# Optimization experiments

Hardware: AMD Instinct MI355X
Metric: run time of the kernel (lower is better)

Reference implementation:

```python
import jax, jax.numpy as jnp
import numpy as np


def _fps(xyz, S):
    """Farthest point sampling over one cloud. xyz: [N,3] -> idx [S] (int32).
    Deterministic start at index 0 (torch_cluster.fps uses a random start; the
    algorithm is otherwise identical)."""
    d0 = jnp.sum((xyz - xyz[0]) ** 2, axis=-1)  # squared dist to first pick

    def step(mind, _):
        nxt = jnp.argmax(mind)                              # farthest from selected set
        d = jnp.sum((xyz - xyz[nxt]) ** 2, axis=-1)
        return jnp.minimum(mind, d), nxt.astype(jnp.int32)

    _, rest = jax.lax.scan(step, d0, None, length=S - 1)
    return jnp.concatenate([jnp.zeros((1,), jnp.int32), rest])


def _gather(points, idx):
    """points [B,N,C], idx [B,...] -> [B,...,C] (per-batch fancy gather)."""
    return jax.vmap(lambda p, i: p[i])(points, idx)


def setup_inputs() -> dict:
    key = jax.random.key(0)
    k1, k2 = jax.random.split(key)
    B, N, C = 8, 4096, 64
    channel_out = C + 3  # use_xyz=True
    return {
        "xyz": jax.random.normal(k1, (B, N, 3), dtype=jnp.float32),
        "points": jax.random.normal(k2, (B, N, C), dtype=jnp.float32),
        "affine_alpha": jnp.ones((1, 1, 1, channel_out), dtype=jnp.float32),
        "affine_beta": jnp.zeros((1, 1, 1, channel_out), dtype=jnp.float32),
        "groups": 1024,
        "kneighbors": 32,
    }


def reference(xyz, points, affine_alpha, affine_beta, groups, kneighbors):
    B, N, _ = xyz.shape
    S, K = groups, kneighbors

    # --- FPS sample S centroids per batch ---
    fps_idx = jax.vmap(lambda x: _fps(x, S))(xyz)              # [B,S]
    new_xyz = _gather(xyz, fps_idx)                            # [B,S,3]
    new_points = _gather(points, fps_idx)                      # [B,S,C]

    # --- KNN: K nearest input points for each centroid ---
    # squared distances [B,S,N] via ||q||^2 + ||x||^2 - 2 q.x
    d2 = (jnp.sum(new_xyz ** 2, -1)[..., None]
          + jnp.sum(xyz ** 2, -1)[:, None, :]
          - 2.0 * jnp.einsum("bsc,bnc->bsn", new_xyz, xyz))
    idx = jax.lax.top_k(-d2, K)[1]                             # [B,S,K]

    grouped_xyz = _gather(xyz, idx)                            # [B,S,K,3]
    grouped_points = _gather(points, idx)                      # [B,S,K,C]
    grouped_points = jnp.concatenate([grouped_points, grouped_xyz], axis=-1)  # use_xyz

    # --- per-group center normalize + global (per-batch) std, affine ---
    mean = jnp.mean(grouped_points, axis=2, keepdims=True)     # [B,S,1,C+3]
    centered = grouped_points - mean
    std = jnp.std(centered.reshape(B, -1), axis=-1, ddof=1)    # unbiased, like torch.std
    std = std[:, None, None, None]
    grouped_points = centered / (std + 1e-5)
    grouped_points = affine_alpha * grouped_points + affine_beta

    new_points_out = jnp.concatenate(
        [grouped_points,
         jnp.broadcast_to(new_points[:, :, None, :], (B, S, K, new_points.shape[-1]))],
        axis=-1)                                               # [B,S,K,2C+3]
    return new_xyz, new_points_out
```

## Files before the change

kernel.cpp:

```cpp
#include <hip/hip_runtime.h>
#include <math.h>

#define NPTS 4096
#define NS 1024
#define NK 32
#define NC 64
#define NCG 67
#define NCOUT 131
#define NB 8
#define GRID 512

typedef float v2f __attribute__((ext_vector_type(2)));
typedef unsigned long long ull;

__device__ __forceinline__ float wave_max_dpp(float v) {
  int x = __float_as_int(v);
#define DPP_STEP(ctrl)                                                        \
  {                                                                           \
    int t = __builtin_amdgcn_update_dpp(x, x, ctrl, 0xF, 0xF, false);         \
    x = __float_as_int(fmaxf(__int_as_float(x), __int_as_float(t)));          \
  }
  DPP_STEP(0x111)
  DPP_STEP(0x112)
  DPP_STEP(0x114)
  DPP_STEP(0x118)
  DPP_STEP(0x142)
  DPP_STEP(0x143)
#undef DPP_STEP
  return __int_as_float(__builtin_amdgcn_readlane(x, 63));
}

__device__ __forceinline__ void wave_argmin_dpp(float& v, int& i) {
#define ARG_STEP(ctrl)                                                         \
  {                                                                            \
    int tv = __builtin_amdgcn_update_dpp(__float_as_int(v), __float_as_int(v), \
                                         ctrl, 0xF, 0xF, false);               \
    int ti = __builtin_amdgcn_update_dpp(i, i, ctrl, 0xF, 0xF, false);         \
    float ov = __int_as_float(tv);                                             \
    bool t = (ov < v) || (ov == v && ti < i);                                  \
    v = t ? ov : v;                                                            \
    i = t ? ti : i;                                                            \
  }
  ARG_STEP(0x111) ARG_STEP(0x112) ARG_STEP(0x114)
  ARG_STEP(0x118) ARG_STEP(0x142) ARG_STEP(0x143)
#undef ARG_STEP
  v = __int_as_float(__builtin_amdgcn_readlane(__float_as_int(v), 63));
  i = __builtin_amdgcn_readlane(i, 63);
}

__device__ __forceinline__ void lds_barrier() {
  asm volatile("s_waitcnt lgkmcnt(0)" ::: "memory");
  __builtin_amdgcn_s_barrier();
  asm volatile("" ::: "memory");
}

__device__ __forceinline__ void unpack4(const float4* __restrict__ X4,
                                        float* px, float* py, float* pz) {
  float4 a = X4[0], c = X4[1], e = X4[2];
  px[0] = a.x; py[0] = a.y; pz[0] = a.z;
  px[1] = a.w; py[1] = c.x; pz[1] = c.y;
  px[2] = c.z; py[2] = c.w; pz[2] = e.x;
  px[3] = e.y; py[3] = e.z; pz[3] = e.w;
}

__device__ __forceinline__ void unpack16(const float4* __restrict__ X4,
                                         float* px, float* py, float* pz) {
#pragma unroll
  for (int g = 0; g < 4; ++g) unpack4(X4 + 3 * g, px + 4 * g, py + 4 * g, pz + 4 * g);
}

__global__ __launch_bounds__(256) void fused_kernel(const float* __restrict__ xyz,
                                                    const float* __restrict__ points,
                                                    float* __restrict__ newxyz,
                                                    int* __restrict__ fps_idx,
                                                    int* __restrict__ knn_idx,
                                                    float* __restrict__ mean_ws,
                                                    float* __restrict__ part_ws,
                                                    int* pick_idx) {
  __shared__ float4 coords4[NPTS];
  __shared__ int fps_lds[NS];
  __shared__ ull keys[2][4];
  __shared__ float pvv[2][4];
  __shared__ int pii[2][4];
  __shared__ int idx_lds[NK];
  __shared__ float red[256];
  __shared__ int gi_sh;

  const int tid = threadIdx.x;
  const int lane = tid & 63;
  const int wav = tid >> 6;
  const int bx = blockIdx.x;

  if (bx < NB) {
#pragma clang fp contract(off)
    __builtin_amdgcn_s_setprio(3);
    const int b = bx;
    const float* X = xyz + (size_t)b * NPTS * 3;
    const int base = tid * 16;
    float px[16], py[16], pz[16];
    unpack16((const float4*)(X + (size_t)base * 3), px, py, pz);
#pragma unroll
    for (int j = 0; j < 16; ++j) coords4[base + j] = make_float4(px[j], py[j], pz[j], 0.0f);
    v2f px2[8], py2[8], pz2[8], mind2[8];
#pragma unroll
    for (int q = 0; q < 8; ++q) {
      px2[q] = v2f{px[2 * q], px[2 * q + 1]};
      py2[q] = v2f{py[2 * q], py[2 * q + 1]};
      pz2[q] = v2f{pz[2 * q], pz[2 * q + 1]};
      mind2[q] = v2f{__builtin_inff(), __builtin_inff()};
    }
    float cx = X[0], cy = X[1], cz = X[2];
    int gi = 0;
    if (tid == 0) fps_lds[0] = 0;
    __syncthreads();

    for (int s = 1; s < NS; ++s) {
      v2f cxv = v2f{cx, cx}, cyv = v2f{cy, cy}, czv = v2f{cz, cz};
      v2f runmax = v2f{-1.0f, -1.0f};
#pragma unroll
      for (int q = 0; q < 8; ++q) {
        v2f dx = px2[q] - cxv;
        v2f dy = py2[q] - cyv;
        v2f dz = pz2[q] - czv;
        v2f d = ((dx * dx) + (dy * dy)) + (dz * dz);
        v2f m = __builtin_elementwise_min(mind2[q], d);
        mind2[q] = m;
        runmax = __builtin_elementwise_max(runmax, m);
      }
      float bv = fmaxf(runmax.x, runmax.y);
      int bj = 0;
#pragma unroll
      for (int q = 7; q >= 0; --q) {
        bj = (mind2[q].y == bv) ? 2 * q + 1 : bj;
        bj = (mind2[q].x == bv) ? 2 * q : bj;
      }
      float smax = wave_max_dpp(bv);
      ull lm = __ballot(bv == smax);
      int wl = (int)(__ffsll(lm) - 1);
      int bjw = __builtin_amdgcn_readlane(bj, wl);
      int gidx = ((wav << 6) + wl) * 16 + bjw;
      ull key = ((ull)__float_as_uint(smax) << 32) |
                (ull)(0xFFFFFFFFu - (unsigned)gidx);
      const int p = s & 1;
      if (lane == 0) keys[p][wav] = key;
      lds_barrier();
      ull k0 = keys[p][0], k1 = keys[p][1], k2 = keys[p][2], k3 = keys[p][3];
      ull ka = k0 > k1 ? k0 : k1;
      ull kb = k2 > k3 ? k2 : k3;
      ull km = ka > kb ? ka : kb;
      gi = (int)(0xFFFFFFFFu - (unsigned)(km & 0xFFFFFFFFull));
      float4 c4 = coords4[gi];
      if (tid == 0) {
        fps_lds[s] = gi;
        __hip_atomic_store(&pick_idx[b * NS + s], gi, __ATOMIC_RELAXED,
                           __HIP_MEMORY_SCOPE_AGENT);
      }
      cx = c4.x; cy = c4.y; cz = c4.z;
    }
    __syncthreads();
    for (int s = tid; s < NS; s += 256) {
      int g2 = fps_lds[s];
      float4 c4 = coords4[g2];
      fps_idx[b * NS + s] = g2;
      newxyz[(size_t)(b * NS + s) * 3 + 0] = c4.x;
      newxyz[(size_t)(b * NS + s) * 3 + 1] = c4.y;
      newxyz[(size_t)(b * NS + s) * 3 + 2] = c4.z;
    }
  } else {
    if (bx >= 256 && bx < 256 + NB) return;
    const int w = (bx < 256) ? (bx - NB) : (bx - NB - NB);
    const int nwork = GRID - 2 * NB;
    for (int q = w; q < NB * NS; q += nwork) {
      const int b = q & 7;
      const int s = q >> 3;
      const int bs = (b << 10) | s;
      int gi = 0;
      if (s != 0) {
        if (tid == 0) {
          int g = __hip_atomic_load(&pick_idx[bs], __ATOMIC_RELAXED,
                                    __HIP_MEMORY_SCOPE_AGENT);
          while (g == -1) {
            __builtin_amdgcn_s_sleep(64);
            g = __hip_atomic_load(&pick_idx[bs], __ATOMIC_RELAXED,
                                  __HIP_MEMORY_SCOPE_AGENT);
          }
          gi_sh = g;
        }
        __syncthreads();
        gi = gi_sh;
      }
      const float* X = xyz + (size_t)b * NPTS * 3;
      const float sx = X[gi * 3 + 0];
      const float sy = X[gi * 3 + 1];
      const float sz = X[gi * 3 + 2];
      const float snorm = __fadd_rn(__fadd_rn(__fmul_rn(sx, sx), __fmul_rn(sy, sy)),
                                    __fmul_rn(sz, sz));
      const int base = tid * 16;
      const float4* X4 = (const float4*)(X + (size_t)base * 3);
      float d2[16];
      float bv = __builtin_inff(); int bi = 0x7fffffff;
#pragma unroll
      for (int g4 = 0; g4 < 4; ++g4) {
        float qx[4], qy[4], qz[4];
        unpack4(X4 + 3 * g4, qx, qy, qz);
#pragma unroll
        for (int j = 0; j < 4; ++j) {
          const int jj = 4 * g4 + j;
          float nn = __fadd_rn(__fadd_rn(__fmul_rn(qx[j], qx[j]), __fmul_rn(qy[j], qy[j])),
                               __fmul_rn(qz[j], qz[j]));
          float dt = __fmaf_rn(sz, qz[j], __fmaf_rn(sy, qy[j], __fmul_rn(sx, qx[j])));
          float d = __fsub_rn(__fadd_rn(snorm, nn), __fmul_rn(2.0f, dt));
          d2[jj] = d;
          if (d < bv) { bv = d; bi = base + jj; }
        }
      }
      float wv = bv; int wi = bi;
      wave_argmin_dpp(wv, wi);
      for (int k = 0; k < NK; ++k) {
        const int p = k & 1;
        if ((tid & 63) == 0) { pvv[p][wav] = wv; pii[p][wav] = wi; }
        __syncthreads();
        float gv = pvv[p][0]; int g2 = pii[p][0];
#pragma unroll
        for (int ww = 1; ww < 4; ++ww) {
          float ov = pvv[p][ww]; int oi = pii[p][ww];
          bool t = (ov < gv) || (ov == gv && oi < g2);
          if (t) { gv = ov; g2 = oi; }
        }
        if (tid == 0) idx_lds[k] = g2;
        if ((g2 >> 10) == wav) {
          if ((g2 >> 4) == tid) {
            bv = __builtin_inff(); bi = 0x7fffffff;
#pragma unroll
            for (int j = 0; j < 16; ++j) {
              float d = d2[j];
              if (base + j == g2) { d = __builtin_inff(); d2[j] = d; }
              if (d < bv) { bv = d; bi = base + j; }
            }
          }
          wv = bv; wi = bi;
          wave_argmin_dpp(wv, wi);
        }
      }
      __syncthreads();
      if (tid < NK) knn_idx[(size_t)bs * NK + tid] = idx_lds[tid];
      float acc = 0.0f;
      if (tid < NCG) {
        const float* Pb = points + (size_t)b * NPTS * NC;
        const float* Xb = xyz + (size_t)b * NPTS * 3;
        float sum = 0.0f, sumsq = 0.0f;
#pragma unroll
        for (int k = 0; k < NK; ++k) {
          int row = idx_lds[k];
          float g = (tid < NC) ? Pb[(size_t)row * NC + tid] : Xb[(size_t)row * 3 + (tid - NC)];
          sum += g;
          sumsq = __fmaf_rn(g, g, sumsq);
        }
        float m = sum * (1.0f / 32.0f);
        mean_ws[(size_t)bs * NCG + tid] = m;
        acc = __fmaf_rn(-m, sum, sumsq);
      }
      red[tid] = acc;
      __syncthreads();
      for (int off = 128; off > 0; off >>= 1) {
        if (tid < off) red[tid] += red[tid + off];
        __syncthreads();
      }
      if (tid == 0) part_ws[bs] = red[0];
      __syncthreads();
    }
  }
}

__global__ __launch_bounds__(256) void scale_kernel(const float* __restrict__ part_ws,
                                                    float* __restrict__ scale_ws) {
  const int b = blockIdx.x;
  const int tid = threadIdx.x;
  __shared__ float red[256];
  const float* p = part_ws + (size_t)b * NS;
  float a = p[tid] + p[tid + 256] + p[tid + 512] + p[tid + 768];
  red[tid] = a;
  __syncthreads();
  for (int off = 128; off > 0; off >>= 1) {
    if (tid < off) red[tid] += red[tid + off];
    __syncthreads();
  }
  if (tid == 0) {
    float var = red[0] / 2195455.0f;
    scale_ws[b] = 1.0f / (sqrtf(var) + 1e-5f);
  }
}

__global__ __launch_bounds__(256) void out_kernel(const float* __restrict__ xyz,
                                                  const float* __restrict__ points,
                                                  const float* __restrict__ alpha,
                                                  const float* __restrict__ beta,
                                                  const int* __restrict__ fps_idx,
                                                  const int* __restrict__ knn_idx,
                                                  const float* __restrict__ mean_ws,
                                                  const float* __restrict__ scale_ws,
                                                  float* __restrict__ out2) {
  const int bs = blockIdx.x;
  const int b = bs >> 10;
  const int tid = threadIdx.x;
  __shared__ int idx[NK];
  __shared__ float mrow[NCG], al[NCG], be[NCG];
  __shared__ int fr_s;
  if (tid < NK) idx[tid] = knn_idx[(size_t)bs * NK + tid];
  if (tid < NCG) {
    mrow[tid] = mean_ws[(size_t)bs * NCG + tid];
    al[tid] = alpha[tid];
    be[tid] = beta[tid];
  }
  if (tid == 0) fr_s = fps_idx[bs];
  __syncthreads();
  const float scl = scale_ws[b];
  const int fr = fr_s;
  const float* Pb = points + (size_t)b * NPTS * NC;
  const float* Xb = xyz + (size_t)b * NPTS * 3;
  float* orow = out2 + (size_t)bs * NK * NCOUT;
  const float* Fr = Pb + (size_t)fr * NC;
  for (int e4 = tid; e4 < NK * NCOUT / 4; e4 += 256) {
    float4 v4;
    float* vp = &v4.x;
#pragma unroll
    for (int j = 0; j < 4; ++j) {
      int e = 4 * e4 + j;
      int k = e / NCOUT;
      int c = e - k * NCOUT;
      float v;
      if (c < NCG) {
        int row = idx[k];
        float gv = (c < NC) ? Pb[(size_t)row * NC + c] : Xb[(size_t)row * 3 + (c - NC)];
        v = (gv - mrow[c]) * scl * al[c] + be[c];
      } else {
        v = Fr[c - NCG];
      }
      vp[j] = v;
    }
    ((float4*)orow)[e4] = v4;
  }
}

extern "C" void kernel_launch(void* const* d_in, const int* in_sizes, int n_in,
                              void* d_out, int out_size, void* d_ws, size_t ws_size,
                              hipStream_t stream) {
  const float* xyz    = (const float*)d_in[0];
  const float* points = (const float*)d_in[1];
  const float* alpha  = (const float*)d_in[2];
  const float* beta   = (const float*)d_in[3];

  float* out = (float*)d_out;
  float* newxyz = out;
  float* out2 = out + (size_t)NB * NS * 3;

  char* ws = (char*)d_ws;
  int*   fps_idx  = (int*)(ws + 0);
  int*   knn_idx  = (int*)(ws + 32768);
  float* mean_ws  = (float*)(ws + 1081344);
  float* part_ws  = (float*)(ws + 3276800);
  float* scale_ws = (float*)(ws + 3309568);
  int*   pick_idx = (int*)(ws + 3309632);

  hipMemsetAsync(pick_idx, 0xFF, NB * NS * sizeof(int), stream);

  fused_kernel<<<GRID,    256, 0, stream>>>(xyz, points, newxyz, fps_idx, knn_idx,
                                            mean_ws, part_ws, pick_idx);
  scale_kernel<<<NB,      256, 0, stream>>>(part_ws, scale_ws);
  out_kernel  <<<NB * NS, 256, 0, stream>>>(xyz, points, alpha, beta, fps_idx, knn_idx,
                                            mean_ws, scale_ws, out2);
}
```

Before: 663.1 us.

## Replace per-step FPS workgroup barrier with tagged LDS key polling

Inside the serial FPS loop, the s_barrier after each wave publishes its argmax key is replaced by polling of the four LDS key slots. A parity tag bit in each key marks which iteration wrote it, so waves only wait for the data they need instead of a full workgroup barrier. The gather worker mapping also skips blocks 8-15, presumably to keep more CUs or slots free near the FPS blocks. The spin loop depends on relaxed LDS atomics being seen in order, and the smaller index field limits gidx to 31 bits.

```diff
diff --git a/kernel.cpp b/kernel.cpp
--- a/kernel.cpp
+++ b/kernel.cpp
@@ -46,12 +46,6 @@
 #undef ARG_STEP
   v = __int_as_float(__builtin_amdgcn_readlane(__float_as_int(v), 63));
   i = __builtin_amdgcn_readlane(i, 63);
-}
-
-__device__ __forceinline__ void lds_barrier() {
-  asm volatile("s_waitcnt lgkmcnt(0)" ::: "memory");
-  __builtin_amdgcn_s_barrier();
-  asm volatile("" ::: "memory");
 }
 
 __device__ __forceinline__ void unpack4(const float4* __restrict__ X4,
@@ -112,6 +106,10 @@
     float cx = X[0], cy = X[1], cz = X[2];
     int gi = 0;
     if (tid == 0) fps_lds[0] = 0;
+    if (tid < 4) {
+      keys[0][tid] = 0ull;
+      keys[1][tid] = (ull)0x80000000u;
+    }
     __syncthreads();
 
     for (int s = 1; s < NS; ++s) {
@@ -139,16 +137,27 @@
       int wl = (int)(__ffsll(lm) - 1);
       int bjw = __builtin_amdgcn_readlane(bj, wl);
       int gidx = ((wav << 6) + wl) * 16 + bjw;
+      const int p = s & 1;
+      const unsigned tag = ((unsigned)(s >> 1) & 1u) << 31;
       ull key = ((ull)__float_as_uint(smax) << 32) |
-                (ull)(0xFFFFFFFFu - (unsigned)gidx);
-      const int p = s & 1;
-      if (lane == 0) keys[p][wav] = key;
-      lds_barrier();
-      ull k0 = keys[p][0], k1 = keys[p][1], k2 = keys[p][2], k3 = keys[p][3];
+                (ull)(tag | (0x7FFFFFFFu - (unsigned)gidx));
+      if (lane == 0)
+        __hip_atomic_store(&keys[p][wav], key, __ATOMIC_RELAXED,
+                           __HIP_MEMORY_SCOPE_WORKGROUP);
+      ull k0, k1, k2, k3;
+      for (;;) {
+        k0 = __hip_atomic_load(&keys[p][0], __ATOMIC_RELAXED, __HIP_MEMORY_SCOPE_WORKGROUP);
+        k1 = __hip_atomic_load(&keys[p][1], __ATOMIC_RELAXED, __HIP_MEMORY_SCOPE_WORKGROUP);
+        k2 = __hip_atomic_load(&keys[p][2], __ATOMIC_RELAXED, __HIP_MEMORY_SCOPE_WORKGROUP);
+        k3 = __hip_atomic_load(&keys[p][3], __ATOMIC_RELAXED, __HIP_MEMORY_SCOPE_WORKGROUP);
+        unsigned nr = (((unsigned)k0 ^ tag) | ((unsigned)k1 ^ tag) |
+                       ((unsigned)k2 ^ tag) | ((unsigned)k3 ^ tag)) & 0x80000000u;
+        if (!nr) break;
+      }
       ull ka = k0 > k1 ? k0 : k1;
       ull kb = k2 > k3 ? k2 : k3;
       ull km = ka > kb ? ka : kb;
-      gi = (int)(0xFFFFFFFFu - (unsigned)(km & 0xFFFFFFFFull));
+      gi = (int)(0x7FFFFFFFu - ((unsigned)km & 0x7FFFFFFFu));
       float4 c4 = coords4[gi];
       if (tid == 0) {
         fps_lds[s] = gi;
@@ -167,9 +176,10 @@
       newxyz[(size_t)(b * NS + s) * 3 + 2] = c4.z;
     }
   } else {
+    if (bx >= 8 && bx < 16) return;
     if (bx >= 256 && bx < 256 + NB) return;
-    const int w = (bx < 256) ? (bx - NB) : (bx - NB - NB);
-    const int nwork = GRID - 2 * NB;
+    const int w = (bx < 256) ? (bx - 16) : (bx - 24);
+    const int nwork = GRID - 24;
     for (int q = w; q < NB * NS; q += nwork) {
       const int b = q & 7;
       const int s = q >> 3;
```

Measured after the change: 669.8 us. No clear change (+1.0%).
